# Performance work log

Measured on AMD Instinct MI355X. Metric: run time of the kernel, lower is better.

The kernel has to match this reference:

```python
import jax, jax.numpy as jnp
import numpy as np

N = 262144      # total nodes in disjoint batch
E = 4194304     # total edges (COO)
G = 4096        # number of graphs
DIN = 1
CH = 32


def setup_inputs() -> dict:
    key = jax.random.key(0)
    ks = jax.random.split(key, 16)
    inp = {
        "x": jax.random.uniform(ks[0], (N, DIN), dtype=jnp.float32),
        "edge_src": jax.random.randint(ks[1], (E,), 0, N, dtype=jnp.int32),
        "edge_dst": jax.random.randint(ks[2], (E,), 0, N, dtype=jnp.int32),
        "edge_w": jax.random.uniform(ks[3], (E,), dtype=jnp.float32),  # normalized-adj values
        "seg": jnp.sort(jax.random.randint(ks[4], (N,), 0, G, dtype=jnp.int32)),
        "W1_1": jax.random.normal(ks[5], (DIN, CH), dtype=jnp.float32) * 0.5,
        "W2_1": jax.random.normal(ks[6], (DIN, CH), dtype=jnp.float32) * 0.5,
        "b1": jnp.zeros((CH,), jnp.float32),
        "W1_2": jax.random.normal(ks[7], (CH, CH), dtype=jnp.float32) * (1.0 / np.sqrt(CH)),
        "W2_2": jax.random.normal(ks[8], (CH, CH), dtype=jnp.float32) * (1.0 / np.sqrt(CH)),
        "b2": jnp.zeros((CH,), jnp.float32),
        "W1_3": jax.random.normal(ks[9], (CH, CH), dtype=jnp.float32) * (1.0 / np.sqrt(CH)),
        "W2_3": jax.random.normal(ks[10], (CH, CH), dtype=jnp.float32) * (1.0 / np.sqrt(CH)),
        "b3": jnp.zeros((CH,), jnp.float32),
        "Wd": jax.random.normal(ks[11], (CH, 1), dtype=jnp.float32) * (1.0 / np.sqrt(CH)),
        "bd": jnp.zeros((1,), jnp.float32),
    }
    return inp


def gcs_conv(x, src, dst, w, W1, W2, b):
    # GCSConv: out = relu(A_hat @ (x W1) + x W2 + b), A_hat sparse COO
    h = x @ W1                                   # [N, CH]
    msg = h[src] * w[:, None]                    # gather + edge weight [E, CH]
    agg = jax.ops.segment_sum(msg, dst, num_segments=N)  # scatter-add [N, CH]
    return jax.nn.relu(agg + x @ W2 + b)


def reference(x, edge_src, edge_dst, edge_w, seg,
              W1_1, W2_1, b1, W1_2, W2_2, b2, W1_3, W2_3, b3, Wd, bd):
    x = gcs_conv(x, edge_src, edge_dst, edge_w, W1_1, W2_1, b1)
    x = gcs_conv(x, edge_src, edge_dst, edge_w, W1_2, W2_2, b2)
    x = gcs_conv(x, edge_src, edge_dst, edge_w, W1_3, W2_3, b3)
    # GlobalAvgPool over graph segments
    sums = jax.ops.segment_sum(x, seg, num_segments=G)           # [G, CH]
    counts = jax.ops.segment_sum(jnp.ones((x.shape[0],), x.dtype), seg, num_segments=G)
    pooled = sums / jnp.maximum(counts, 1.0)[:, None]            # [G, CH]
    return jax.nn.sigmoid(pooled @ Wd + bd)                      # [G, 1]
```

## Files before the change

### kernel.cpp

```cpp
#include <hip/hip_runtime.h>
#include <hip/hip_bf16.h>
#include <hip/hip_fp8.h>

#define CH 32
#define BSHIFT 10
#define BNODES (1 << BSHIFT)
#define MAXBUK 256
#define P3_CHUNK 8192
#define NT 32
#define CAP 1024

__device__ __forceinline__ float fp8_to_f32(unsigned int b) {
    __hip_fp8_e4m3 v; v.__x = (__hip_fp8_storage_t)b; return (float)v;
}
__device__ __forceinline__ unsigned char f32_to_fp8(float f) {
    return (unsigned char)__hip_fp8_e4m3(f).__x;
}


__global__ void bucket_hist_kernel(const int* __restrict__ dst, int* __restrict__ bucketCount,
                                   int E, int nbuk) {
    __shared__ int h[MAXBUK];
    int tid = threadIdx.x;
    if (tid < nbuk) h[tid] = 0;
    __syncthreads();
    int stride = gridDim.x * blockDim.x;
    for (int e = blockIdx.x * blockDim.x + tid; e < E; e += stride)
        atomicAdd(&h[dst[e] >> BSHIFT], 1);
    __syncthreads();
    if (tid < nbuk && h[tid]) atomicAdd(&bucketCount[tid], h[tid]);
}

__global__ void bucket_scan_kernel(const int* __restrict__ bucketCount, int* __restrict__ bucketStart,
                                   int* __restrict__ bucketTail, int* __restrict__ row_start,
                                   int nbuk, int N, int E) {
    __shared__ int l[MAXBUK];
    int tid = threadIdx.x;
    int v = (tid < nbuk) ? bucketCount[tid] : 0;
    l[tid] = v;
    __syncthreads();
    for (int off = 1; off < MAXBUK; off <<= 1) {
        int t = (tid >= off) ? l[tid - off] : 0;
        __syncthreads();
        l[tid] += t;
        __syncthreads();
    }
    int ex = l[tid] - v;
    if (tid < nbuk) { bucketStart[tid] = ex; bucketTail[tid] = ex; }
    if (tid == nbuk - 1) bucketStart[nbuk] = ex + v;
    if (tid == 0) row_start[N] = E;
}

__global__ void bucket_scatter_kernel(const int* __restrict__ src, const int* __restrict__ dst,
                                      const float* __restrict__ w, int* __restrict__ bucketTail,
                                      int2* __restrict__ rec, int E, int nbuk) {
    __shared__ int cnt[MAXBUK], base[MAXBUK], offs[MAXBUK];
    int tid = threadIdx.x;
    int begin = blockIdx.x * P3_CHUNK;
    int end = min(begin + P3_CHUNK, E);
    if (tid < nbuk) cnt[tid] = 0;
    __syncthreads();
    for (int e = begin + tid; e < end; e += 256)
        atomicAdd(&cnt[dst[e] >> BSHIFT], 1);
    __syncthreads();
    if (tid < nbuk) {
        base[tid] = cnt[tid] ? atomicAdd(&bucketTail[tid], cnt[tid]) : 0;
        offs[tid] = 0;
    }
    __syncthreads();
    for (int e = begin + tid; e < end; e += 256) {
        int d = dst[e];
        int b = d >> BSHIFT;
        int p = base[b] + atomicAdd(&offs[b], 1);
        rec[p] = make_int2(src[e] | ((d & (BNODES - 1)) << 18), __float_as_int(w[e]));
    }
}

__global__ void local_csr_kernel(const int2* __restrict__ rec, const int* __restrict__ bucketStart,
                                 int* __restrict__ row_start, int2* __restrict__ colw, int N) {
    int b = blockIdx.x;
    int lo = bucketStart[b], hi = bucketStart[b + 1];
    int nodeBase = b << BSHIFT;
    int nNodes = min(BNODES, N - nodeBase);
    __shared__ int deg[BNODES];
    __shared__ int rs[BNODES];
    __shared__ int l[256];
    int tid = threadIdx.x;
    for (int i = tid; i < BNODES; i += 256) deg[i] = 0;
    __syncthreads();
    for (int j = lo + tid; j < hi; j += 256)
        atomicAdd(&deg[rec[j].x >> 18], 1);
    __syncthreads();
    int i0 = tid * 4;
    int v0 = deg[i0], v1 = deg[i0 + 1], v2 = deg[i0 + 2], v3 = deg[i0 + 3];
    int tsum = v0 + v1 + v2 + v3;
    l[tid] = tsum;
    __syncthreads();
    for (int off = 1; off < 256; off <<= 1) {
        int t = (tid >= off) ? l[tid - off] : 0;
        __syncthreads();
        l[tid] += t;
        __syncthreads();
    }
    int ex = l[tid] - tsum;
    rs[i0] = ex; rs[i0 + 1] = ex + v0; rs[i0 + 2] = ex + v0 + v1; rs[i0 + 3] = ex + v0 + v1 + v2;
    __syncthreads();
    for (int i = tid; i < nNodes; i += 256) row_start[nodeBase + i] = lo + rs[i];
    for (int i = tid; i < BNODES; i += 256) deg[i] = 0;
    __syncthreads();
    for (int j = lo + tid; j < hi; j += 256) {
        int2 r = rec[j];
        int dl = r.x >> 18;
        int p = lo + rs[dl] + atomicAdd(&deg[dl], 1);
        colw[p] = make_int2(r.x & 0x3FFFF, r.y);
    }
}

__global__ void l1_fused_kernel(const float* __restrict__ x,
                                const int* __restrict__ row_start, const int2* __restrict__ colw,
                                const float* __restrict__ W11, const float* __restrict__ W21,
                                const float* __restrict__ b1, const float* __restrict__ W12,
                                float* __restrict__ x1, unsigned char* __restrict__ h2, int N) {
    __shared__ float w1s[CH][CH];
    __shared__ float xs[8][CH + 1];
    int tid = threadIdx.x;
    for (int t = tid; t < CH * CH; t += 256) w1s[t >> 5][t & 31] = W12[t];
    int ln = tid >> 5, c = tid & 31;
    int node = blockIdx.x * 8 + ln;
    float s = 0.f, xv = 0.f;
    if (node < N) {
        xv = x[node];
        int lo = row_start[node], hi = row_start[node + 1];
        for (int j = lo + c; j < hi; j += 32) {
            int2 cw = colw[j];
            s += __int_as_float(cw.y) * x[cw.x];
        }
    }
    for (int m = 1; m < 32; m <<= 1) s += __shfl_xor(s, m);
    float x1v = 0.f;
    if (node < N) {
        x1v = fmaxf(fmaf(s, W11[c], fmaf(xv, W21[c], b1[c])), 0.f);
        x1[(size_t)node * CH + c] = x1v;
    }
    xs[ln][c] = x1v;
    __syncthreads();
    if (node < N) {
        float a = 0.f;
#pragma unroll
        for (int k = 0; k < CH; k++) a = fmaf(xs[ln][k], w1s[k][c], a);
        h2[(size_t)node * CH + c] = f32_to_fp8(a);
    }
}

template <bool EMIT_H>
__global__ void gather_kernel(float* __restrict__ xio, const unsigned char* __restrict__ h,
                              const int* __restrict__ row_start, const int2* __restrict__ colw,
                              const float* __restrict__ W2, const float* __restrict__ b,
                              const float* __restrict__ W1next, unsigned char* __restrict__ hout,
                              int N) {
    __shared__ float w2s[CH][CH];
    __shared__ float w1s[EMIT_H ? CH : 1][CH];
    __shared__ float xs[NT][CH + 1];
    __shared__ int2 cws[CAP];
    int tid = threadIdx.x;
    int nodeBase = blockIdx.x * NT;

    for (int t = tid; t < CH * CH; t += 256) {
        w2s[t >> 5][t & 31] = W2[t];
        if (EMIT_H) w1s[t >> 5][t & 31] = W1next[t];
    }
    {
        int n = tid >> 5, c = tid & 31;
        for (int p = 0; p < NT / 8; p++) {
            int node = nodeBase + p * 8 + n;
            xs[p * 8 + n][c] = (node < N) ? xio[(size_t)node * CH + c] : 0.f;
        }
    }
    int lo = row_start[min(nodeBase, N)];
    int hi = row_start[min(nodeBase + NT, N)];
    int cnt = min(hi - lo, CAP);
    for (int t = tid; t < cnt; t += 256) cws[t] = colw[lo + t];
    __syncthreads();

    int grp = tid >> 4, l16 = tid & 15;
    int c0 = l16 * 2;
#pragma unroll
    for (int rep = 0; rep < NT / 16; rep++) {
        int nloc = rep * 16 + grp;
        int node = nodeBase + nloc;
        if (node < N) {
            int ls = row_start[node], le = row_start[node + 1];
            float a0 = b[c0], a1 = b[c0 + 1];
#pragma unroll
            for (int k = 0; k < CH; k++) {
                float xk = xs[nloc][k];
                float2 wk = *reinterpret_cast<const float2*>(&w2s[k][c0]);
                a0 = fmaf(xk, wk.x, a0);
                a1 = fmaf(xk, wk.y, a1);
            }
            if (le - lo <= cnt) {
                int j = ls;
                for (; j + 4 <= le; j += 4) {
                    int2 e0 = cws[j - lo], e1 = cws[j + 1 - lo], e2 = cws[j + 2 - lo], e3 = cws[j + 3 - lo];
                    unsigned int p0 = *reinterpret_cast<const unsigned short*>(h + (size_t)e0.x * CH + c0);
                    unsigned int p1 = *reinterpret_cast<const unsigned short*>(h + (size_t)e1.x * CH + c0);
                    unsigned int p2 = *reinterpret_cast<const unsigned short*>(h + (size_t)e2.x * CH + c0);
                    unsigned int p3 = *reinterpret_cast<const unsigned short*>(h + (size_t)e3.x * CH + c0);
                    float w0 = __int_as_float(e0.y), w1 = __int_as_float(e1.y);
                    float w2 = __int_as_float(e2.y), w3 = __int_as_float(e3.y);
                    a0 = fmaf(w0, fp8_to_f32(p0 & 0xff), a0); a1 = fmaf(w0, fp8_to_f32(p0 >> 8), a1);
                    a0 = fmaf(w1, fp8_to_f32(p1 & 0xff), a0); a1 = fmaf(w1, fp8_to_f32(p1 >> 8), a1);
                    a0 = fmaf(w2, fp8_to_f32(p2 & 0xff), a0); a1 = fmaf(w2, fp8_to_f32(p2 >> 8), a1);
                    a0 = fmaf(w3, fp8_to_f32(p3 & 0xff), a0); a1 = fmaf(w3, fp8_to_f32(p3 >> 8), a1);
                }
                for (; j < le; j++) {
                    int2 e = cws[j - lo];
                    unsigned int p = *reinterpret_cast<const unsigned short*>(h + (size_t)e.x * CH + c0);
                    float wj = __int_as_float(e.y);
                    a0 = fmaf(wj, fp8_to_f32(p & 0xff), a0); a1 = fmaf(wj, fp8_to_f32(p >> 8), a1);
                }
            } else {
                for (int j = ls; j < le; j++) {
                    int2 e = colw[j];
                    unsigned int p = *reinterpret_cast<const unsigned short*>(h + (size_t)e.x * CH + c0);
                    float wj = __int_as_float(e.y);
                    a0 = fmaf(wj, fp8_to_f32(p & 0xff), a0); a1 = fmaf(wj, fp8_to_f32(p >> 8), a1);
                }
            }
            float r0 = fmaxf(a0, 0.f), r1 = fmaxf(a1, 0.f);
            *reinterpret_cast<float2*>(&xio[(size_t)node * CH + c0]) = make_float2(r0, r1);
            if (EMIT_H) { xs[nloc][c0] = r0; xs[nloc][c0 + 1] = r1; }
        }
    }
    if (EMIT_H) {
        __syncthreads();
#pragma unroll
        for (int rep = 0; rep < NT / 16; rep++) {
            int nloc = rep * 16 + grp;
            int node = nodeBase + nloc;
            if (node >= N) continue;
            float a0 = 0.f, a1 = 0.f;
#pragma unroll
            for (int k = 0; k < CH; k++) {
                float xk = xs[nloc][k];
                float2 wk = *reinterpret_cast<const float2*>(&w1s[k][c0]);
                a0 = fmaf(xk, wk.x, a0);
                a1 = fmaf(xk, wk.y, a1);
            }
            unsigned short pk = (unsigned short)f32_to_fp8(a0) |
                                ((unsigned short)f32_to_fp8(a1) << 8);
            *reinterpret_cast<unsigned short*>(hout + (size_t)node * CH + c0) = pk;
        }
    }
}

__global__ void pool_head_kernel(const float* __restrict__ x3, const int* __restrict__ seg,
                                 const float* __restrict__ Wd, const float* __restrict__ bd,
                                 float* __restrict__ out, int N, int G) {
    int g = blockIdx.x;
    int tid = threadIdx.x;
    int lo = 0, hi = N;
    while (lo < hi) { int mid = (lo + hi) >> 1; if (seg[mid] < g) lo = mid + 1; else hi = mid; }
    int start = lo;
    hi = N;
    while (lo < hi) { int mid = (lo + hi) >> 1; if (seg[mid] < g + 1) lo = mid + 1; else hi = mid; }
    int end = lo;
    int half = tid >> 5, c = tid & 31;
    float s = 0.f;
    for (int n = start + half; n < end; n += 2) s += x3[(size_t)n * CH + c];
    s += __shfl_xor(s, 32);
    float t = s * Wd[c];
    for (int m = 1; m < 32; m <<= 1) t += __shfl_xor(t, m);
    if (tid == 0) {
        float cnt = fmaxf((float)(end - start), 1.f);
        float logit = t / cnt + bd[0];
        out[g] = 1.f / (1.f + expf(-logit));
    }
}

extern "C" void kernel_launch(void* const* d_in, const int* in_sizes, int n_in,
                              void* d_out, int out_size, void* d_ws, size_t ws_size,
                              hipStream_t stream) {
    const float* x        = (const float*)d_in[0];
    const int*   edge_src = (const int*)d_in[1];
    const int*   edge_dst = (const int*)d_in[2];
    const float* edge_w   = (const float*)d_in[3];
    const int*   seg      = (const int*)d_in[4];
    const float* W1_1 = (const float*)d_in[5];
    const float* W2_1 = (const float*)d_in[6];
    const float* b1   = (const float*)d_in[7];
    const float* W1_2 = (const float*)d_in[8];
    const float* W2_2 = (const float*)d_in[9];
    const float* b2   = (const float*)d_in[10];
    const float* W1_3 = (const float*)d_in[11];
    const float* W2_3 = (const float*)d_in[12];
    const float* b3   = (const float*)d_in[13];
    const float* Wd   = (const float*)d_in[14];
    const float* bd   = (const float*)d_in[15];
    float* out = (float*)d_out;

    const int N = in_sizes[0];
    const int E = in_sizes[1];
    const int G = out_size;
    (void)ws_size; (void)n_in;

    const int nbuk = (N + BNODES - 1) >> BSHIFT;

    const size_t NB = (size_t)N * CH;
    float*           xbuf      = (float*)d_ws;
    int2*            rec       = (int2*)d_ws;
    unsigned char*   h8a       = (unsigned char*)(xbuf + NB);
    unsigned char*   h8b       = h8a + NB;
    int*             row_start = (int*)(h8b + NB);
    int2*            colw      = (int2*)(row_start + (N + 8));
    int*             bucketCount = (int*)(colw + E);
    int*             bucketStart = bucketCount + MAXBUK;
    int*             bucketTail  = bucketStart + MAXBUK + 4;

    const int BLK = 256;

    hipMemsetAsync(bucketCount, 0, MAXBUK * sizeof(int), stream);
    bucket_hist_kernel<<<512, BLK, 0, stream>>>(edge_dst, bucketCount, E, nbuk);
    bucket_scan_kernel<<<1, BLK, 0, stream>>>(bucketCount, bucketStart, bucketTail, row_start, nbuk, N, E);
    bucket_scatter_kernel<<<(E + P3_CHUNK - 1) / P3_CHUNK, BLK, 0, stream>>>(
        edge_src, edge_dst, edge_w, bucketTail, rec, E, nbuk);
    local_csr_kernel<<<nbuk, BLK, 0, stream>>>(rec, bucketStart, row_start, colw, N);

    l1_fused_kernel<<<(N + 7) / 8, BLK, 0, stream>>>(x, row_start, colw,
                                                     W1_1, W2_1, b1, W1_2, xbuf, h8a, N);
    gather_kernel<true><<<(N + NT - 1) / NT, BLK, 0, stream>>>(xbuf, h8a, row_start, colw,
                                                               W2_2, b2, W1_3, h8b, N);
    gather_kernel<false><<<(N + NT - 1) / NT, BLK, 0, stream>>>(xbuf, h8b, row_start, colw,
                                                                W2_3, b3, nullptr, nullptr, N);

    pool_head_kernel<<<G, 64, 0, stream>>>(xbuf, seg, Wd, bd, out, N, G);
}
```

Before: 411.7 us.

## Stage bucket scatter in shared memory for coalesced writes; shrink chunk and edge cache

The bucket scatter kernel now sorts each chunk's records by bucket in shared memory, using a local prefix scan, and then writes them out contiguously per bucket. This replaces random per-edge global writes with mostly coalesced runs. The chunk size drops from 8192 to 2048 so the staging buffer fits in LDS, which means more blocks and more global atomics on the bucket tails. The conv kernel's edge cache shrinks to 768 entries and its cache-hit check becomes a per-block test, so blocks with more edges than that take the fallback path entirely.

```diff
diff --git a/kernel.cpp b/kernel.cpp
--- a/kernel.cpp
+++ b/kernel.cpp
@@ -6,9 +6,9 @@
 #define BSHIFT 10
 #define BNODES (1 << BSHIFT)
 #define MAXBUK 256
-#define P3_CHUNK 8192
+#define P3_CHUNK 2048
 #define NT 32
-#define CAP 1024
+#define CAP 768
 
 __device__ __forceinline__ float fp8_to_f32(unsigned int b) {
     __hip_fp8_e4m3 v; v.__x = (__hip_fp8_storage_t)b; return (float)v;
@@ -54,25 +54,46 @@
 __global__ void bucket_scatter_kernel(const int* __restrict__ src, const int* __restrict__ dst,
                                       const float* __restrict__ w, int* __restrict__ bucketTail,
                                       int2* __restrict__ rec, int E, int nbuk) {
-    __shared__ int cnt[MAXBUK], base[MAXBUK], offs[MAXBUK];
+    __shared__ int cnt[MAXBUK], lstart[MAXBUK], base[MAXBUK], offs[MAXBUK];
+    __shared__ int l[MAXBUK];
+    __shared__ int2 stage[P3_CHUNK];
     int tid = threadIdx.x;
     int begin = blockIdx.x * P3_CHUNK;
     int end = min(begin + P3_CHUNK, E);
-    if (tid < nbuk) cnt[tid] = 0;
+    int m = end - begin;
+    if (tid < MAXBUK) cnt[tid] = 0;
     __syncthreads();
     for (int e = begin + tid; e < end; e += 256)
         atomicAdd(&cnt[dst[e] >> BSHIFT], 1);
     __syncthreads();
+    int v = (tid < nbuk) ? cnt[tid] : 0;
+    l[tid] = v;
+    __syncthreads();
+    for (int off = 1; off < MAXBUK; off <<= 1) {
+        int t = (tid >= off) ? l[tid - off] : 0;
+        __syncthreads();
+        l[tid] += t;
+        __syncthreads();
+    }
     if (tid < nbuk) {
-        base[tid] = cnt[tid] ? atomicAdd(&bucketTail[tid], cnt[tid]) : 0;
+        lstart[tid] = l[tid] - v;
         offs[tid] = 0;
+        base[tid] = v ? atomicAdd(&bucketTail[tid], v) : 0;
     }
     __syncthreads();
     for (int e = begin + tid; e < end; e += 256) {
         int d = dst[e];
         int b = d >> BSHIFT;
-        int p = base[b] + atomicAdd(&offs[b], 1);
-        rec[p] = make_int2(src[e] | ((d & (BNODES - 1)) << 18), __float_as_int(w[e]));
+        int p = lstart[b] + atomicAdd(&offs[b], 1);
+        stage[p] = make_int2(src[e] | ((d & (BNODES - 1)) << 18), __float_as_int(w[e]));
+    }
+    __syncthreads();
+    for (int t = tid; t < m; t += 256) {
+        int b = 0;
+#pragma unroll
+        for (int s = 128; s; s >>= 1)
+            if (b + s <= nbuk - 1 && lstart[b + s] <= t) b += s;
+        rec[base[b] + (t - lstart[b])] = stage[t];
     }
 }
 
@@ -178,7 +199,8 @@
     }
     int lo = row_start[min(nodeBase, N)];
     int hi = row_start[min(nodeBase + NT, N)];
-    int cnt = min(hi - lo, CAP);
+    int total = hi - lo;
+    int cnt = min(total, CAP);
     for (int t = tid; t < cnt; t += 256) cws[t] = colw[lo + t];
     __syncthreads();
 
@@ -198,7 +220,7 @@
                 a0 = fmaf(xk, wk.x, a0);
                 a1 = fmaf(xk, wk.y, a1);
             }
-            if (le - lo <= cnt) {
+            if (total <= cnt) {
                 int j = ls;
                 for (; j + 4 <= le; j += 4) {
                     int2 e0 = cws[j - lo], e1 = cws[j + 1 - lo], e2 = cws[j + 2 - lo], e3 = cws[j + 3 - lo];
@@ -267,13 +289,13 @@
     int end = lo;
     int half = tid >> 5, c = tid & 31;
     float s = 0.f;
-    for (int n = start + half; n < end; n += 2) s += x3[(size_t)n * CH + c];
+    for (int nn = start + half; nn < end; nn += 2) s += x3[(size_t)nn * CH + c];
     s += __shfl_xor(s, 32);
     float t = s * Wd[c];
     for (int m = 1; m < 32; m <<= 1) t += __shfl_xor(t, m);
     if (tid == 0) {
-        float cnt = fmaxf((float)(end - start), 1.f);
-        float logit = t / cnt + bd[0];
+        float cntf = fmaxf((float)(end - start), 1.f);
+        float logit = t / cntf + bd[0];
         out[g] = 1.f / (1.f + expf(-logit));
     }
 }
```

Result: slower. 440.8 us (+7.1%).
